# Kernel tuning notes

Measured on AMD Instinct MI355X. Metric: run time of the kernel, lower is better.

## Reference

```python
import jax, jax.numpy as jnp
import numpy as np

ALPHA = 0.15  # top-k fraction (forward default)


def setup_inputs() -> dict:
    key = jax.random.key(0)
    k1, k2, k3 = jax.random.split(key, 3)
    B, N, D = 8, 1024, 256
    x = jax.random.normal(k1, (B, N, D), dtype=jnp.float32)
    # torch nn.Linear(dim, H*head_dim, bias=False); stored here as [D, H*head_dim]
    W_src = jax.random.normal(k2, (D, D), dtype=jnp.float32) * (1.0 / np.sqrt(D))
    W_tgt = jax.random.normal(k3, (D, D), dtype=jnp.float32) * (1.0 / np.sqrt(D))
    return {"x": x, "W_src": W_src, "W_tgt": W_tgt}


def _topk_mask(adj, k):
    # adj: [B,H,N,N]; exact scatter of 1.0 at top-k indices along last axis
    B, H, N, _ = adj.shape
    _, idx = jax.lax.top_k(adj, k)              # [B,H,N,k]
    bi = jnp.arange(B)[:, None, None, None]
    hi = jnp.arange(H)[None, :, None, None]
    ni = jnp.arange(N)[None, None, :, None]
    mask = jnp.zeros_like(adj).at[bi, hi, ni, idx].set(1.0)
    return mask


def reference(x, W_src, W_tgt):
    # directed=True path of DirectedGraphLearner.forward
    B, N, D = x.shape
    H, head_dim = 4, D // 4
    k = max(1, int(ALPHA * N))
    src = (x @ W_src).reshape(B, N, H, head_dim)
    tgt = (x @ W_tgt).reshape(B, N, H, head_dim)
    adj = jnp.einsum('bihd,bjhd->bhij', src, tgt)
    adj = jax.nn.gelu(adj, approximate=False)    # torch F.gelu default = exact erf
    mask = _topk_mask(adj, k)
    return adj * mask
```

## Files before the change

### kernel.cpp

```cpp
#include <hip/hip_runtime.h>
#include <math.h>


#define KSEL 153u
#define EPSK 61000u
#define EPSKS 76000u

typedef __attribute__((ext_vector_type(8))) short short8v;
typedef __attribute__((ext_vector_type(4))) float float4v;

__device__ __forceinline__ float gelu_f32(float x) {
    return 0.5f * x * (1.0f + erff(x * 0.70710678118654752f));
}

__device__ __forceinline__ unsigned long long d2key(double v) {
    unsigned long long u = (unsigned long long)__double_as_longlong(v);
    return (u >> 63) ? ~u : (u | 0x8000000000000000ull);
}

__device__ __forceinline__ unsigned lkeyf(float v) {
    float q = fmaf(v, 33554432.0f, 2147483648.0f);
    q = fminf(fmaxf(q, 0.0f), 4294967040.0f);
    return (unsigned)q;
}

__device__ __forceinline__ unsigned short b16(float x) {
    unsigned u = __float_as_uint(x);
    u += 0x7FFFu + ((u >> 16) & 1u);
    return (unsigned short)(u >> 16);
}
__device__ __forceinline__ float bf2f(unsigned short h) {
    return __uint_as_float(((unsigned)h) << 16);
}
__device__ __forceinline__ unsigned pk2(float a, float b) {
    return (unsigned)b16(a) | ((unsigned)b16(b) << 16);
}

#define LGKM0()                                             \
    do {                                                    \
        asm volatile("s_waitcnt lgkmcnt(0)" ::: "memory");  \
        __builtin_amdgcn_sched_barrier(0);                  \
    } while (0)

template <bool W32>
__global__ __launch_bounds__(256) void k1_proj(const float* __restrict__ x,
                                               const float* __restrict__ Wsrc,
                                               const float* __restrict__ Wtgt,
                                               double* __restrict__ ws,
                                               unsigned short* __restrict__ th,
                                               unsigned short* __restrict__ tl) {
    __shared__ float xs[32 * 68];
    __shared__ float wsh[32 * 68];
    const int t = threadIdx.x;
    const int bx = blockIdx.x;
    const int by = blockIdx.y;
    const int col0 = (by & 3) * 64;
    const float* __restrict__ W = (by < 4) ? Wsrc : Wtgt;
    double* __restrict__ outp = ws + ((by < 4) ? 0 : 2097152);

    double acc[4][4];
#pragma unroll
    for (int i = 0; i < 4; ++i)
#pragma unroll
        for (int j = 0; j < 4; ++j) acc[i][j] = 0.0;

    const int m_loc = (t & 15) * 4;
    const int c_loc = (t >> 4) * 4;

    for (int kt = 0; kt < 8; ++kt) {
        __syncthreads();
#pragma unroll
        for (int it = 0; it < 2; ++it) {
            int f4 = t + 256 * it;
            int m = f4 >> 3, k4 = f4 & 7;
            float4 v = *reinterpret_cast<const float4*>(&x[(bx * 64 + m) * 256 + kt * 32 + 4 * k4]);
            xs[(4 * k4 + 0) * 68 + m] = v.x;
            xs[(4 * k4 + 1) * 68 + m] = v.y;
            xs[(4 * k4 + 2) * 68 + m] = v.z;
            xs[(4 * k4 + 3) * 68 + m] = v.w;
        }
#pragma unroll
        for (int it = 0; it < 2; ++it) {
            int f4 = t + 256 * it;
            int k = f4 >> 4, c4 = f4 & 15;
            *reinterpret_cast<float4*>(&wsh[k * 68 + 4 * c4]) =
                *reinterpret_cast<const float4*>(&W[(kt * 32 + k) * 256 + col0 + 4 * c4]);
        }
        __syncthreads();
#pragma unroll
        for (int kk = 0; kk < 32; ++kk) {
            float4 a = *reinterpret_cast<const float4*>(&xs[kk * 68 + m_loc]);
            float4 b = *reinterpret_cast<const float4*>(&wsh[kk * 68 + c_loc]);
            double ad[4] = {a.x, a.y, a.z, a.w};
            double bd[4] = {b.x, b.y, b.z, b.w};
#pragma unroll
            for (int i = 0; i < 4; ++i)
#pragma unroll
                for (int j = 0; j < 4; ++j) acc[i][j] += ad[i] * bd[j];
        }
    }
    const int hd = by & 3;
#pragma unroll
    for (int i = 0; i < 4; ++i) {
        int m = bx * 64 + m_loc + i;
        int b = m >> 10, n = m & 1023;
        int bhd = b * 4 + hd;
        size_t base = ((size_t)(bhd * 1024 + n)) * 64 + c_loc;
        double2 v01, v23;
        v01.x = acc[i][0]; v01.y = acc[i][1];
        v23.x = acc[i][2]; v23.y = acc[i][3];
        *reinterpret_cast<double2*>(&outp[base]) = v01;
        *reinterpret_cast<double2*>(&outp[base + 2]) = v23;
        if (W32 && by >= 4) {
            float f0 = (float)acc[i][0], f1 = (float)acc[i][1];
            float f2 = (float)acc[i][2], f3 = (float)acc[i][3];
            unsigned short h0 = b16(f0), h1 = b16(f1), h2 = b16(f2), h3 = b16(f3);
            uint2 H, L;
            H.x = (unsigned)h0 | ((unsigned)h1 << 16);
            H.y = (unsigned)h2 | ((unsigned)h3 << 16);
            L.x = pk2(f0 - bf2f(h0), f1 - bf2f(h1));
            L.y = pk2(f2 - bf2f(h2), f3 - bf2f(h3));
            int T = n >> 4, colLow = n & 15;
            int ks = c_loc >> 5, kg = (c_loc >> 3) & 3, elem = c_loc & 7;
            size_t fidx = ((size_t)bhd * 65536) +
                          (size_t)(((T * 2 + ks) * 64 + kg * 16 + colLow) * 8 + elem);
            *reinterpret_cast<uint2*>(&th[fidx]) = H;
            *reinterpret_cast<uint2*>(&tl[fidx]) = L;
        }
    }
}

template <bool FAST, bool S16>
__global__ __launch_bounds__(256, 4) void k2a_gemm(const double* __restrict__ srcT,
                                                   const double* __restrict__ tgtT,
                                                   const unsigned short* __restrict__ th,
                                                   const unsigned short* __restrict__ tlo,
                                                   short* __restrict__ adjS,
                                                   float* __restrict__ out) {
    __shared__ __align__(16) float tr[16 * 512];

    unsigned short* sHI = reinterpret_cast<unsigned short*>(tr);
    unsigned short* sLO = sHI + 1024;

    const int t = threadIdx.x;
    const int lane = t & 63;
    const int wv = t >> 6;
    const int bid = (blockIdx.x & 7) * 256 + (blockIdx.x >> 3);
    const int bh = bid >> 6;
    const int itile = bid & 63;
    const int row0 = itile * 16;
    const int r0 = 4 * wv;
    const size_t tgtBase = (size_t)bh * 65536;
    const unsigned short* __restrict__ thb = th + tgtBase;
    const unsigned short* __restrict__ tlb = tlo + tgtBase;

    {
        int r = t >> 4, dq = (t & 15) * 4;
        const double* sp = &srcT[((size_t)bh * 1024 + row0 + r) * 64 + dq];
        double2 a = *reinterpret_cast<const double2*>(sp);
        double2 b = *reinterpret_cast<const double2*>(sp + 2);
        float f0 = (float)a.x, f1 = (float)a.y, f2 = (float)b.x, f3 = (float)b.y;
        unsigned short h0 = b16(f0), h1 = b16(f1), h2 = b16(f2), h3 = b16(f3);
        int s = dq >> 3;
        int idx = r * 64 + ((s ^ (r & 7)) << 3) + (dq & 7);
        uint2 H, L;
        H.x = (unsigned)h0 | ((unsigned)h1 << 16);
        H.y = (unsigned)h2 | ((unsigned)h3 << 16);
        L.x = pk2(f0 - bf2f(h0), f1 - bf2f(h1));
        L.y = pk2(f2 - bf2f(h2), f3 - bf2f(h3));
        *reinterpret_cast<uint2*>(&sHI[idx]) = H;
        *reinterpret_cast<uint2*>(&sLO[idx]) = L;
    }
    __syncthreads();

    short8v Ah[2], Al[2];
#pragma unroll
    for (int ks = 0; ks < 2; ++ks) {
        int idxA = (lane & 15) * 64 + (((4 * ks + (lane >> 4)) ^ (lane & 7)) << 3);
        Ah[ks] = *reinterpret_cast<const short8v*>(&sHI[idxA]);
        Al[ks] = *reinterpret_cast<const short8v*>(&sLO[idxA]);
    }

    const int colA = lane & 15;
    const int kgrp = lane >> 4;
    const size_t rowG0 = (size_t)bh * 1024 + row0 + r0;

#pragma unroll
    for (int h = 0; h < 2; ++h) {
        float4v acc[8];
#pragma unroll
        for (int a = 0; a < 8; ++a) acc[a] = (float4v){0.f, 0.f, 0.f, 0.f};

#pragma unroll
        for (int u = 0; u < 8; ++u) {
            const int T = 32 * h + 4 * u + wv;
#pragma unroll
            for (int ks = 0; ks < 2; ++ks) {
                short8v Bh, Bl;
                if (FAST) {
                    const size_t fbase = (size_t)(((T * 2 + ks) * 64 + lane) * 8);
                    Bh = *reinterpret_cast<const short8v*>(&thb[fbase]);
                    Bl = *reinterpret_cast<const short8v*>(&tlb[fbase]);
                } else {
                    const size_t cbase = (size_t)(16 * T + colA) * 64 + kgrp * 8;
                    const double* gp = &tgtT[tgtBase + cbase + 32 * ks];
                    double2 d0 = *reinterpret_cast<const double2*>(gp);
                    double2 d1 = *reinterpret_cast<const double2*>(gp + 2);
                    double2 d2 = *reinterpret_cast<const double2*>(gp + 4);
                    double2 d3 = *reinterpret_cast<const double2*>(gp + 6);
                    float f[8] = {(float)d0.x, (float)d0.y, (float)d1.x, (float)d1.y,
                                  (float)d2.x, (float)d2.y, (float)d3.x, (float)d3.y};
                    unsigned short hh[8];
#pragma unroll
                    for (int e = 0; e < 8; ++e) hh[e] = b16(f[e]);
                    unsigned Hw[4], Lw[4];
#pragma unroll
                    for (int e = 0; e < 4; ++e) {
                        Hw[e] = (unsigned)hh[2 * e] | ((unsigned)hh[2 * e + 1] << 16);
                        Lw[e] = pk2(f[2 * e] - bf2f(hh[2 * e]), f[2 * e + 1] - bf2f(hh[2 * e + 1]));
                    }
                    Bh = *reinterpret_cast<const short8v*>(Hw);
                    Bl = *reinterpret_cast<const short8v*>(Lw);
                }
                acc[u] = __builtin_amdgcn_mfma_f32_16x16x32_bf16(Ah[ks], Bh, acc[u], 0, 0, 0);
                acc[u] = __builtin_amdgcn_mfma_f32_16x16x32_bf16(Al[ks], Bh, acc[u], 0, 0, 0);
                acc[u] = __builtin_amdgcn_mfma_f32_16x16x32_bf16(Ah[ks], Bl, acc[u], 0, 0, 0);
            }
        }

        __syncthreads();
#pragma unroll
        for (int u = 0; u < 8; ++u) {
            int colh = 16 * (4 * u + wv) + colA;
#pragma unroll
            for (int reg = 0; reg < 4; ++reg) {
                int row = 4 * kgrp + reg;
                tr[row * 512 + (colh ^ ((kgrp & 1) << 4))] = acc[u][reg];
            }
        }
        __syncthreads();
        const int rsw = (wv & 1) << 4;
#pragma unroll
        for (int ri = 0; ri < 4; ++ri) {
            int row = r0 + ri;
#pragma unroll
            for (int q = 0; q < 2; ++q) {
                int colh = 4 * lane + 256 * q;
                float4 v = *reinterpret_cast<const float4*>(&tr[row * 512 + (colh ^ rsw)]);
                if (S16) {
                    short4 s;
                    s.x = (short)__float2int_rn(fminf(fmaxf(v.x * 512.f, -32767.f), 32767.f));
                    s.y = (short)__float2int_rn(fminf(fmaxf(v.y * 512.f, -32767.f), 32767.f));
                    s.z = (short)__float2int_rn(fminf(fmaxf(v.z * 512.f, -32767.f), 32767.f));
                    s.w = (short)__float2int_rn(fminf(fmaxf(v.w * 512.f, -32767.f), 32767.f));
                    *reinterpret_cast<short4*>(&adjS[(rowG0 + ri) * 1024 + 512 * h + colh]) = s;
                } else {
                    *reinterpret_cast<float4*>(&out[(rowG0 + ri) * 1024 + 512 * h + colh]) = v;
                }
            }
        }
    }
}

template <bool S16>
__global__ __launch_bounds__(256, 4) void k2b_select(const double* __restrict__ srcT,
                                                     const double* __restrict__ tgtT,
                                                     const short* __restrict__ adjS,
                                                     float* __restrict__ out) {
    __shared__ __align__(16) unsigned hist[4][256];

    const int t = threadIdx.x;
    const int lane = t & 63;
    const int wv = t >> 6;
    const int R = blockIdx.x * 4 + wv;
    const int bh = R >> 10;
    const size_t tgtBase = (size_t)bh * 65536;
    const size_t base = (size_t)R * 1024;
    const unsigned eps = S16 ? EPSKS : EPSK;

    float vals[16];
    if (S16) {
#pragma unroll
        for (int q = 0; q < 2; ++q) {
            short8v s = *reinterpret_cast<const short8v*>(&adjS[base + 16 * lane + 8 * q]);
#pragma unroll
            for (int e = 0; e < 8; ++e) vals[8 * q + e] = (float)s[e] * (1.0f / 512.0f);
        }
    } else {
#pragma unroll
        for (int q = 0; q < 4; ++q) {
            float4 v = *reinterpret_cast<const float4*>(&out[base + 16 * lane + 4 * q]);
            vals[4 * q + 0] = v.x;
            vals[4 * q + 1] = v.y;
            vals[4 * q + 2] = v.z;
            vals[4 * q + 3] = v.w;
        }
    }

    unsigned* histw = hist[wv];
    unsigned* cjp = histw + 128;
    unsigned long long* ckp = reinterpret_cast<unsigned long long*>(histw);
    unsigned* ccp = histw + 192;

    unsigned ul[16];
#pragma unroll
    for (int m = 0; m < 16; ++m) ul[m] = lkeyf(vals[m]);

    unsigned prefA = 0u, maskA = 0u, rk = KSEL;
#pragma unroll 1
    for (int p = 1; p >= 0; --p) {
        const int sh = 16 + 8 * p;
        *reinterpret_cast<uint4*>(&histw[4 * lane]) = make_uint4(0u, 0u, 0u, 0u);
        LGKM0();
#pragma unroll
        for (int m = 0; m < 16; ++m) {
            if ((ul[m] & maskA) == prefA)
                atomicAdd(&histw[(ul[m] >> sh) & 255u], 1u);
        }
        LGKM0();
        unsigned h0 = histw[4 * lane + 0], h1 = histw[4 * lane + 1];
        unsigned h2 = histw[4 * lane + 2], h3 = histw[4 * lane + 3];
        unsigned S = h0 + h1 + h2 + h3;
        unsigned inc = S;
#pragma unroll
        for (int off = 1; off < 64; off <<= 1) {
            unsigned o = __shfl_down(inc, off, 64);
            inc = (lane + off < 64) ? (inc + o) : inc;
        }
        unsigned above = inc - S;
        bool found = (above < rk) && (rk <= inc);
        unsigned long long bal = __ballot(found);
        int L = __ffsll(bal) - 1;
        unsigned hh[4];
        hh[0] = __shfl(h0, L, 64);
        hh[1] = __shfl(h1, L, 64);
        hh[2] = __shfl(h2, L, 64);
        hh[3] = __shfl(h3, L, 64);
        unsigned cum = __shfl(above, L, 64);
        int bsel = -1;
#pragma unroll
        for (int q = 3; q >= 0; --q) {
            if (bsel < 0) {
                if (rk <= cum + hh[q]) {
                    bsel = q;
                    rk = rk - cum;
                } else {
                    cum += hh[q];
                }
            }
        }
        prefA |= (unsigned)(4 * L + bsel) << sh;
        maskA |= 0xFFu << sh;
    }

    const unsigned klo = prefA - eps;
    const unsigned khi = prefA + 65535u + eps;

    int ch = 0, cb = 0;
#pragma unroll
    for (int m = 0; m < 16; ++m) {
        ch += (ul[m] > khi) ? 1 : 0;
        cb += (ul[m] >= klo && ul[m] <= khi) ? 1 : 0;
    }
#pragma unroll
    for (int off = 32; off; off >>= 1) {
        ch += __shfl_xor(ch, off, 64);
        cb += __shfl_xor(cb, off, 64);
    }
    const unsigned need = KSEL - (unsigned)ch;
    const bool fastp = ((unsigned)cb == need);

    unsigned long long selMask = 0ull;
    unsigned cidx[16];
    if (!fastp) {
        if (lane == 0) *ccp = 0u;
        LGKM0();
#pragma unroll
        for (int m = 0; m < 16; ++m) {
            cidx[m] = 0xFFFFFFFFu;
            if (ul[m] >= klo && ul[m] <= khi) {
                unsigned idx = atomicAdd(ccp, 1u);
                cidx[m] = idx;
                if (idx < 64u) cjp[idx] = (unsigned)(16 * lane + m);
            }
        }
        LGKM0();
        unsigned g = *ccp;
        if (g > 64u) g = 64u;
        unsigned rnk = need;
        if (lane < (int)g) {
            unsigned j = cjp[lane];
            const double2* sp = reinterpret_cast<const double2*>(&srcT[(size_t)R * 64]);
            const double2* tp = reinterpret_cast<const double2*>(&tgtT[tgtBase + (size_t)j * 64]);
            double a2 = 0.0;
#pragma unroll 8
            for (int d2 = 0; d2 < 32; ++d2) {
                double2 aa = sp[d2], bb = tp[d2];
                a2 = fma(aa.x, bb.x, fma(aa.y, bb.y, a2));
            }
            ckp[lane] = d2key(a2);
        }
        LGKM0();
        unsigned rnk2 = need;
        if (lane < (int)g) {
            unsigned long long myk = ckp[lane];
            unsigned myj = cjp[lane];
            rnk2 = 0;
            for (unsigned i = 0; i < g; ++i) {
                unsigned long long ki = ckp[i];
                rnk2 += (ki > myk || (ki == myk && cjp[i] < myj)) ? 1u : 0u;
            }
        }
        selMask = __ballot(lane < (int)g && rnk2 < need);
    }

#pragma unroll
    for (int q = 0; q < 4; ++q) {
        float4 o;
        float* op = &o.x;
#pragma unroll
        for (int e = 0; e < 4; ++e) {
            int m = 4 * q + e;
            bool sel;
            if (ul[m] > khi) sel = true;
            else if (ul[m] < klo) sel = false;
            else sel = fastp ? true
                             : ((cidx[m] < 64u) ? (((selMask >> cidx[m]) & 1ull) != 0ull) : false);
            float v = vals[m];
            op[e] = sel ? ((v > 3.0f) ? v : gelu_f32(v)) : 0.0f;
        }
        *reinterpret_cast<float4*>(&out[base + 16 * lane + 4 * q]) = o;
    }
}

extern "C" void kernel_launch(void* const* d_in, const int* in_sizes, int n_in,
                              void* d_out, int out_size, void* d_ws, size_t ws_size,
                              hipStream_t stream) {
    const float* x = (const float*)d_in[0];
    const float* Wsrc = (const float*)d_in[1];
    const float* Wtgt = (const float*)d_in[2];
    float* out = (float*)d_out;
    double* ws = (double*)d_ws;
    unsigned short* th = (unsigned short*)((char*)d_ws + 33554432);
    unsigned short* tl = (unsigned short*)((char*)d_ws + 37748736);
    short* adjS = (short*)((char*)d_ws + 41943040);

    const bool fast = (ws_size >= 40u * 1024u * 1024u);
    const bool s16 = (ws_size >= 104u * 1024u * 1024u);
    dim3 g1(128, 8);
    if (fast && s16) {
        k1_proj<true><<<g1, 256, 0, stream>>>(x, Wsrc, Wtgt, ws, th, tl);
        k2a_gemm<true, true><<<2048, 256, 0, stream>>>(ws, ws + 2097152, th, tl, adjS, out);
        k2b_select<true><<<8192, 256, 0, stream>>>(ws, ws + 2097152, adjS, out);
    } else if (fast) {
        k1_proj<true><<<g1, 256, 0, stream>>>(x, Wsrc, Wtgt, ws, th, tl);
        k2a_gemm<true, false><<<2048, 256, 0, stream>>>(ws, ws + 2097152, th, tl, adjS, out);
        k2b_select<false><<<8192, 256, 0, stream>>>(ws, ws + 2097152, adjS, out);
    } else {
        k1_proj<false><<<g1, 256, 0, stream>>>(x, Wsrc, Wtgt, ws, th, tl);
        k2a_gemm<false, false><<<2048, 256, 0, stream>>>(ws, ws + 2097152, th, tl, adjS, out);
        k2b_select<false><<<8192, 256, 0, stream>>>(ws, ws + 2097152, adjS, out);
    }
}
```

Baseline: 155.6 us.

## Replace two-pass 8-bit radix select with single-pass 1024-bin histogram

The per-row top-k threshold search now builds one 1024-bin LDS histogram from the top 10 key bits, instead of two dependent passes over 256-bin histograms. That removes a histogram clear, an atomic pass and a prefix scan per row. The price is a much coarser bucket, so the epsilon band around the threshold is widened to a single constant. The exact fp64 recompute path will likely be taken more often, and candidates may exceed the 64-slot buffer. Launch bounds go from 4 to 5 blocks per CU, and per-block LDS grows to 16 KB.

```diff
diff --git a/kernel.cpp b/kernel.cpp
--- a/kernel.cpp
+++ b/kernel.cpp
@@ -3,8 +3,7 @@
 
 
 #define KSEL 153u
-#define EPSK 61000u
-#define EPSKS 76000u
+#define EPSX 140000u
 
 typedef __attribute__((ext_vector_type(8))) short short8v;
 typedef __attribute__((ext_vector_type(4))) float float4v;
@@ -263,11 +262,11 @@
 }
 
 template <bool S16>
-__global__ __launch_bounds__(256, 4) void k2b_select(const double* __restrict__ srcT,
+__global__ __launch_bounds__(256, 5) void k2b_select(const double* __restrict__ srcT,
                                                      const double* __restrict__ tgtT,
                                                      const short* __restrict__ adjS,
                                                      float* __restrict__ out) {
-    __shared__ __align__(16) unsigned hist[4][256];
+    __shared__ __align__(16) unsigned hist[4][1024];
 
     const int t = threadIdx.x;
     const int lane = t & 63;
@@ -276,7 +275,6 @@
     const int bh = R >> 10;
     const size_t tgtBase = (size_t)bh * 65536;
     const size_t base = (size_t)R * 1024;
-    const unsigned eps = S16 ? EPSKS : EPSK;
 
     float vals[16];
     if (S16) {
@@ -298,63 +296,51 @@
     }
 
     unsigned* histw = hist[wv];
-    unsigned* cjp = histw + 128;
-    unsigned long long* ckp = reinterpret_cast<unsigned long long*>(histw);
-    unsigned* ccp = histw + 192;
-
     unsigned ul[16];
 #pragma unroll
     for (int m = 0; m < 16; ++m) ul[m] = lkeyf(vals[m]);
 
-    unsigned prefA = 0u, maskA = 0u, rk = KSEL;
-#pragma unroll 1
-    for (int p = 1; p >= 0; --p) {
-        const int sh = 16 + 8 * p;
-        *reinterpret_cast<uint4*>(&histw[4 * lane]) = make_uint4(0u, 0u, 0u, 0u);
-        LGKM0();
-#pragma unroll
-        for (int m = 0; m < 16; ++m) {
-            if ((ul[m] & maskA) == prefA)
-                atomicAdd(&histw[(ul[m] >> sh) & 255u], 1u);
-        }
-        LGKM0();
-        unsigned h0 = histw[4 * lane + 0], h1 = histw[4 * lane + 1];
-        unsigned h2 = histw[4 * lane + 2], h3 = histw[4 * lane + 3];
-        unsigned S = h0 + h1 + h2 + h3;
-        unsigned inc = S;
-#pragma unroll
-        for (int off = 1; off < 64; off <<= 1) {
-            unsigned o = __shfl_down(inc, off, 64);
-            inc = (lane + off < 64) ? (inc + o) : inc;
-        }
-        unsigned above = inc - S;
-        bool found = (above < rk) && (rk <= inc);
-        unsigned long long bal = __ballot(found);
-        int L = __ffsll(bal) - 1;
-        unsigned hh[4];
-        hh[0] = __shfl(h0, L, 64);
-        hh[1] = __shfl(h1, L, 64);
-        hh[2] = __shfl(h2, L, 64);
-        hh[3] = __shfl(h3, L, 64);
-        unsigned cum = __shfl(above, L, 64);
-        int bsel = -1;
-#pragma unroll
-        for (int q = 3; q >= 0; --q) {
-            if (bsel < 0) {
-                if (rk <= cum + hh[q]) {
-                    bsel = q;
-                    rk = rk - cum;
-                } else {
-                    cum += hh[q];
-                }
-            }
-        }
-        prefA |= (unsigned)(4 * L + bsel) << sh;
-        maskA |= 0xFFu << sh;
-    }
-
-    const unsigned klo = prefA - eps;
-    const unsigned khi = prefA + 65535u + eps;
+#pragma unroll
+    for (int e = 0; e < 4; ++e)
+        *reinterpret_cast<uint4*>(&histw[16 * lane + 4 * e]) = make_uint4(0u, 0u, 0u, 0u);
+    LGKM0();
+#pragma unroll
+    for (int m = 0; m < 16; ++m) atomicAdd(&histw[ul[m] >> 22], 1u);
+    LGKM0();
+
+    unsigned h[16];
+#pragma unroll
+    for (int e = 0; e < 4; ++e) {
+        uint4 hv = *reinterpret_cast<const uint4*>(&histw[16 * lane + 4 * e]);
+        h[4 * e + 0] = hv.x; h[4 * e + 1] = hv.y; h[4 * e + 2] = hv.z; h[4 * e + 3] = hv.w;
+    }
+    unsigned S = 0;
+#pragma unroll
+    for (int e = 0; e < 16; ++e) S += h[e];
+    unsigned inc = S;
+#pragma unroll
+    for (int off = 1; off < 64; off <<= 1) {
+        unsigned o = __shfl_down(inc, off, 64);
+        inc = (lane + off < 64) ? (inc + o) : inc;
+    }
+    unsigned above = inc - S;
+    bool found = (above < KSEL) && (KSEL <= inc);
+    unsigned long long bal = __ballot(found);
+    int L = __ffsll(bal) - 1;
+    int bq = 0;
+    {
+        unsigned cum = above;
+#pragma unroll
+        for (int q = 15; q >= 0; --q) {
+            bool hit = (KSEL <= cum + h[q]);
+            if (hit && bq == 0) bq = 16 * lane + q + 1;
+            if (!hit) cum += h[q];
+        }
+    }
+    const unsigned B = (unsigned)(__shfl(bq, L, 64) - 1);
+
+    const unsigned klo = (B << 22) - EPSX;
+    const unsigned khi = ((B + 1) << 22) - 1u + EPSX;
 
     int ch = 0, cb = 0;
 #pragma unroll
@@ -369,6 +355,10 @@
     }
     const unsigned need = KSEL - (unsigned)ch;
     const bool fastp = ((unsigned)cb == need);
+
+    unsigned long long* ckp = reinterpret_cast<unsigned long long*>(histw);
+    unsigned* cjp = histw + 128;
+    unsigned* ccp = histw + 192;
 
     unsigned long long selMask = 0ull;
     unsigned cidx[16];
@@ -387,7 +377,6 @@
         LGKM0();
         unsigned g = *ccp;
         if (g > 64u) g = 64u;
-        unsigned rnk = need;
         if (lane < (int)g) {
             unsigned j = cjp[lane];
             const double2* sp = reinterpret_cast<const double2*>(&srcT[(size_t)R * 64]);
```

Result: slower. 176.9 us (+13.7%).
